# Kernel tuning notes

Measured on AMD Instinct MI355X. Metric: run time of the kernel, lower is better.

The kernel has to match this reference:

```python
import jax, jax.numpy as jnp
import numpy as np

FEATURE_DIM = 256
HEADS = 8


def setup_inputs() -> dict:
    key = jax.random.key(0)
    ks = jax.random.split(key, 9)
    d, h = FEATURE_DIM, HEADS
    b, n = 4, 4096
    s_in = 1.0 / np.sqrt(d)
    s_out = 1.0 / np.sqrt(d * h)
    return {
        "x": jax.random.normal(ks[0], (b, n, d), dtype=jnp.float32),
        "Wq": jax.random.uniform(ks[1], (d, d * h), jnp.float32, -s_in, s_in),
        "bq": jax.random.uniform(ks[2], (d * h,), jnp.float32, -s_in, s_in),
        "Wk": jax.random.uniform(ks[3], (d, d * h), jnp.float32, -s_in, s_in),
        "bk": jax.random.uniform(ks[4], (d * h,), jnp.float32, -s_in, s_in),
        "Wv": jax.random.uniform(ks[5], (d, d * h), jnp.float32, -s_in, s_in),
        "bv": jax.random.uniform(ks[6], (d * h,), jnp.float32, -s_in, s_in),
        "Wo": jax.random.uniform(ks[7], (d * h, d), jnp.float32, -s_out, s_out),
        "bo": jax.random.uniform(ks[8], (d,), jnp.float32, -s_out, s_out),
    }


def reference(x, Wq, bq, Wk, bk, Wv, bv, Wo, bo):
    b, n, d = x.shape
    h = HEADS
    scale = d ** (-0.5)
    # projections: (b, n, h, d) -- note: NO head transpose, matching original
    q = (x @ Wq + bq).reshape(b, n, h, d)
    k = (x @ Wk + bk).reshape(b, n, h, d)
    v = (x @ Wv + bv).reshape(b, n, h, d)
    # attention is head-vs-head per token: (b, n, h, h)
    attn = jnp.einsum("bnhd,bngd->bnhg", q, k) * scale
    attn = jax.nn.softmax(attn, axis=-1)
    out = jnp.einsum("bnhg,bngd->bnhd", attn, v).reshape(b, n, h * d)
    return out @ Wo + bo
```

## Files before the change

### kernel.cpp

```cpp
#include <hip/hip_runtime.h>
#include <hip/hip_bf16.h>
#include <math.h>

typedef __bf16 bf16;
typedef __bf16 bf16x4 __attribute__((ext_vector_type(4)));
typedef __bf16 bf16x8 __attribute__((ext_vector_type(8)));
typedef float f32x4 __attribute__((ext_vector_type(4)));
typedef unsigned int u32;
typedef u32 __attribute__((address_space(1))) gu32;
typedef u32 __attribute__((address_space(3))) lu32;

#define TOK   16384
#define D_    256
#define HD    2048
#define QKVN  6144

#define GLDS16(g, l) __builtin_amdgcn_global_load_lds((gu32*)(g), (lu32*)(l), 16, 0, 0)
#define WAIT_VM(n) __builtin_amdgcn_s_waitcnt(0x0F70 | (n))

__global__ void detect_dtype(const void* __restrict__ x, int* __restrict__ flag)
{
    int lane = threadIdx.x;
    const bf16* xb = (const bf16*)x;
    float m = 0.f;
    for (int i = lane; i < 4096; i += 64) {
        float v = fabsf((float)xb[2 * i]);
        if (!(v < 1e4f)) v = 1e30f;
        m = fmaxf(m, v);
    }
    for (int off = 32; off; off >>= 1) m = fmaxf(m, __shfl_xor(m, off, 64));
    if (lane == 0) *flag = (m > 1e4f) ? 1 : 0;
}

__global__ __launch_bounds__(256) void convert_x(
    const void* __restrict__ src, bf16* __restrict__ dst,
    const int* __restrict__ flag)
{
    int i = blockIdx.x * 256 + threadIdx.x;
    bf16x4 o;
    if (*flag) {
        f32x4 v = ((const f32x4*)src)[i];
        for (int e = 0; e < 4; e++) o[e] = (bf16)v[e];
    } else {
        o = ((const bf16x4*)src)[i];
    }
    ((bf16x4*)dst)[i] = o;
}

__global__ __launch_bounds__(256) void fuse_bias(
    const void* __restrict__ bq, const void* __restrict__ bk,
    const void* __restrict__ bv, const void* __restrict__ bo,
    bf16* __restrict__ bqkv, bf16* __restrict__ bob,
    const int* __restrict__ flag)
{
    int i = blockIdx.x * 256 + threadIdx.x;
    if (i >= 6400) return;
    const void* src; bf16* dst; int off;
    if (i < 2048)      { src = bq; dst = bqkv;        off = i; }
    else if (i < 4096) { src = bk; dst = bqkv + 2048; off = i - 2048; }
    else if (i < 6144) { src = bv; dst = bqkv + 4096; off = i - 4096; }
    else               { src = bo; dst = bob;         off = i - 6144; }
    float v = (*flag) ? ((const float*)src)[off] : (float)((const bf16*)src)[off];
    dst[off] = (bf16)v;
}

__global__ __launch_bounds__(256) void transpose_cvt3(
    const void* __restrict__ Wq, const void* __restrict__ Wk,
    const void* __restrict__ Wv, bf16* __restrict__ WT,
    const int* __restrict__ flag)
{
    __shared__ float tile[32][33];
    int z = blockIdx.z;
    const void* src = (z == 0) ? Wq : (z == 1) ? Wk : Wv;
    bf16* dst = WT + (size_t)z * 2048 * 256;
    int f = *flag;
    int R = 256, C = 2048;
    int tc = blockIdx.x * 32, tr = blockIdx.y * 32;
    int lx = threadIdx.x & 31, ly = threadIdx.x >> 5;
    for (int i = 0; i < 4; i++) {
        int r = ly + i * 8;
        size_t idx = (size_t)(tr + r) * C + tc + lx;
        tile[r][lx] = f ? ((const float*)src)[idx] : (float)((const bf16*)src)[idx];
    }
    __syncthreads();
    for (int i = 0; i < 4; i++) {
        int r = ly + i * 8;
        dst[(size_t)(tc + r) * R + tr + lx] = (bf16)tile[lx][r];
    }
}

__global__ __launch_bounds__(256) void transpose_cvt(
    const void* __restrict__ src, bf16* __restrict__ dst, int R, int C,
    const int* __restrict__ flag)
{
    __shared__ float tile[32][33];
    int f = *flag;
    int tc = blockIdx.x * 32, tr = blockIdx.y * 32;
    int lx = threadIdx.x & 31, ly = threadIdx.x >> 5;
    for (int i = 0; i < 4; i++) {
        int r = ly + i * 8;
        size_t idx = (size_t)(tr + r) * C + tc + lx;
        tile[r][lx] = f ? ((const float*)src)[idx] : (float)((const bf16*)src)[idx];
    }
    __syncthreads();
    for (int i = 0; i < 4; i++) {
        int r = ly + i * 8;
        dst[(size_t)(tc + r) * R + tr + lx] = (bf16)tile[lx][r];
    }
}

__global__ __launch_bounds__(256) void proj_gemm(
    const bf16* __restrict__ X, const bf16* __restrict__ WT,
    const bf16* __restrict__ bqkv, bf16* __restrict__ qkv)
{
    __shared__ char smem[36864];
    bf16* As = (bf16*)smem;
    bf16* Bs = (bf16*)(smem + 16384);
    int m0 = blockIdx.y * 128, n0 = blockIdx.x * 128;
    int tid = threadIdx.x, wave = tid >> 6, lane = tid & 63;
    int wm = (wave >> 1) * 64, wn = (wave & 1) * 64;
    int mrow = lane & 15, quad = lane >> 4;
    int lrow8 = lane >> 3, lslot = lane & 7;

    f32x4 acc[4][4] = {};
    for (int k0 = 0; k0 < D_; k0 += 64) {
        __syncthreads();
        for (int i = 0; i < 4; i++) {
            int rbase = wave * 32 + i * 8;
            int row = rbase + lrow8;
            int gc = lslot ^ (row & 7);
            GLDS16(&X[(size_t)(m0 + row) * D_ + k0 + gc * 8], &As[rbase * 64]);
            GLDS16(&WT[(size_t)(n0 + row) * D_ + k0 + gc * 8], &Bs[rbase * 64]);
        }
        __syncthreads();
        for (int kk = 0; kk < 64; kk += 32) {
            int slot = (((kk >> 3) + quad) ^ (mrow & 7)) * 8;
            bf16x8 af[4], bfv[4];
            for (int mt = 0; mt < 4; mt++)
                af[mt] = *(const bf16x8*)&As[(wm + mt * 16 + mrow) * 64 + slot];
            for (int nt = 0; nt < 4; nt++)
                bfv[nt] = *(const bf16x8*)&Bs[(wn + nt * 16 + mrow) * 64 + slot];
            for (int mt = 0; mt < 4; mt++)
                for (int nt = 0; nt < 4; nt++)
                    acc[mt][nt] = __builtin_amdgcn_mfma_f32_16x16x32_bf16(
                        bfv[nt], af[mt], acc[mt][nt], 0, 0, 0);
        }
    }

    __syncthreads();
    bf16* ep = (bf16*)smem + wave * (64 * 72);
    for (int mt = 0; mt < 4; mt++) {
        for (int nt = 0; nt < 4; nt++) {
            int col = n0 + wn + nt * 16 + quad * 4;
            bf16x4 bb = *(const bf16x4*)&bqkv[col];
            bf16x4 o;
            for (int r = 0; r < 4; r++) o[r] = (bf16)(acc[mt][nt][r] + (float)bb[r]);
            *(bf16x4*)&ep[(mt * 16 + mrow) * 72 + nt * 16 + quad * 4] = o;
        }
    }
    __syncthreads();
    for (int i = 0; i < 8; i++) {
        int r = i * 8 + (lane >> 3);
        int cb = (lane & 7) * 8;
        bf16x8 val = *(const bf16x8*)&ep[r * 72 + cb];
        *(bf16x8*)&qkv[(size_t)(m0 + wm + r) * QKVN + n0 + wn + cb] = val;
    }
}

__global__ __launch_bounds__(256) void attn(bf16* __restrict__ qkv)
{
    __shared__ bf16 sh[4][6144];
    int wave = threadIdx.x >> 6, lane = threadIdx.x & 63;
    bf16* sq = sh[wave];
    int h = lane >> 3, g = lane & 7;
    int wid = blockIdx.x * 4 + wave;
    int start = (wid < 1024) ? wid * 6 : 6144 + (wid - 1024) * 5;
    int count = (wid < 1024) ? 6 : 5;

    for (int ti = 0; ti < count; ti++) {
        int t = start + ti;
        bf16* base = qkv + (size_t)t * QKVN;
        for (int i = 0; i < 12; i++) {
            int s = i * 64 + lane;
            int row = s >> 5, cs = s & 31;
            int gc = cs ^ (row & 7);
            GLDS16(base + row * 256 + gc * 8, (char*)sq + i * 1024);
        }
        WAIT_VM(4);

        const bf16* qrow = sq + h * 256;
        const bf16* krow = sq + (8 + g) * 256;
        float s0 = 0.f, s1 = 0.f, s2 = 0.f, s3 = 0.f;
        for (int c = 0; c < 32; c += 4) {
            bf16x8 a0 = *(const bf16x8*)&qrow[((c + 0) ^ h) * 8];
            bf16x8 b0 = *(const bf16x8*)&krow[((c + 0) ^ g) * 8];
            bf16x8 a1 = *(const bf16x8*)&qrow[((c + 1) ^ h) * 8];
            bf16x8 b1 = *(const bf16x8*)&krow[((c + 1) ^ g) * 8];
            bf16x8 a2 = *(const bf16x8*)&qrow[((c + 2) ^ h) * 8];
            bf16x8 b2 = *(const bf16x8*)&krow[((c + 2) ^ g) * 8];
            bf16x8 a3 = *(const bf16x8*)&qrow[((c + 3) ^ h) * 8];
            bf16x8 b3 = *(const bf16x8*)&krow[((c + 3) ^ g) * 8];
            for (int e = 0; e < 8; e++) {
                s0 += (float)a0[e] * (float)b0[e];
                s1 += (float)a1[e] * (float)b1[e];
                s2 += (float)a2[e] * (float)b2[e];
                s3 += (float)a3[e] * (float)b3[e];
            }
        }
        float s = ((s0 + s1) + (s2 + s3)) * 0.0625f;
        float m = s;
        for (int off = 1; off < 8; off <<= 1) m = fmaxf(m, __shfl_xor(m, off, 8));
        float p = __expf(s - m);
        float sum = p;
        for (int off = 1; off < 8; off <<= 1) sum += __shfl_xor(sum, off, 8);
        p /= sum;

        float pv[8];
        for (int g2 = 0; g2 < 8; g2++) pv[g2] = __shfl(p, h * 8 + g2, 64);

        WAIT_VM(0);

        float acc[4][8] = {};
        for (int g2 = 0; g2 < 8; g2++) {
            float pw = pv[g2];
            const bf16* vrow = sq + (16 + g2) * 256;
            for (int mm = 0; mm < 4; mm++) {
                bf16x8 v = *(const bf16x8*)&vrow[((g ^ g2) + 8 * mm) * 8];
                for (int e = 0; e < 8; e++) acc[mm][e] += pw * (float)v[e];
            }
        }
        bf16* obase = base + h * D_;
        for (int mm = 0; mm < 4; mm++) {
            bf16x8 o;
            for (int e = 0; e < 8; e++) o[e] = (bf16)acc[mm][e];
            *(bf16x8*)&obase[(g + 8 * mm) * 8] = o;
        }
    }
}

__global__ __launch_bounds__(256) void out_gemm(
    const bf16* __restrict__ qkv, const bf16* __restrict__ WoT,
    const bf16* __restrict__ bob, float* __restrict__ outp)
{
    __shared__ bf16 As[64 * 128];
    __shared__ bf16 Bs[128 * 128];
    int m0 = blockIdx.y * 64, n0 = blockIdx.x * 128;
    int tid = threadIdx.x, wave = tid >> 6, lane = tid & 63;
    int wm = (wave >> 1) * 32, wn = (wave & 1) * 64;
    int mrow = lane & 15, quad = lane >> 4;
    int lrow16 = lane >> 4, lslot16 = lane & 15;

    f32x4 acc[2][4] = {};
    for (int k0 = 0; k0 < HD; k0 += 128) {
        __syncthreads();
        for (int i = 0; i < 4; i++) {
            int rbase = wave * 16 + i * 4;
            int row = rbase + lrow16;
            int gc = lslot16 ^ (row & 7);
            GLDS16(&qkv[(size_t)(m0 + row) * QKVN + k0 + gc * 8], &As[rbase * 128]);
        }
        for (int i = 0; i < 8; i++) {
            int rbase = wave * 32 + i * 4;
            int row = rbase + lrow16;
            int gc = lslot16 ^ (row & 7);
            GLDS16(&WoT[(size_t)(n0 + row) * HD + k0 + gc * 8], &Bs[rbase * 128]);
        }
        __syncthreads();
        for (int kk = 0; kk < 128; kk += 32) {
            int slot = (((kk >> 3) + quad) ^ (mrow & 7)) * 8;
            bf16x8 af[2], bfv[4];
            for (int mt = 0; mt < 2; mt++)
                af[mt] = *(const bf16x8*)&As[(wm + mt * 16 + mrow) * 128 + slot];
            for (int nt = 0; nt < 4; nt++)
                bfv[nt] = *(const bf16x8*)&Bs[(wn + nt * 16 + mrow) * 128 + slot];
            for (int mt = 0; mt < 2; mt++)
                for (int nt = 0; nt < 4; nt++)
                    acc[mt][nt] = __builtin_amdgcn_mfma_f32_16x16x32_bf16(
                        bfv[nt], af[mt], acc[mt][nt], 0, 0, 0);
        }
    }

    for (int mt = 0; mt < 2; mt++) {
        int row = m0 + wm + mt * 16 + mrow;
        for (int nt = 0; nt < 4; nt++) {
            int col = n0 + wn + nt * 16 + quad * 4;
            bf16x4 bb = *(const bf16x4*)&bob[col];
            f32x4 o;
            for (int r = 0; r < 4; r++) o[r] = acc[mt][nt][r] + (float)bb[r];
            *(f32x4*)&outp[(size_t)row * D_ + col] = o;
        }
    }
}

extern "C" void kernel_launch(void* const* d_in, const int* in_sizes, int n_in,
                              void* d_out, int out_size, void* d_ws, size_t ws_size,
                              hipStream_t stream)
{
    const void* x  = d_in[0];
    const void* Wq = d_in[1];
    const void* bq = d_in[2];
    const void* Wk = d_in[3];
    const void* bk = d_in[4];
    const void* Wv = d_in[5];
    const void* bv = d_in[6];
    const void* Wo = d_in[7];
    const void* bo = d_in[8];
    float* out = (float*)d_out;

    char* ws = (char*)d_ws;
    bf16* qkv  = (bf16*)ws;
    bf16* WT   = (bf16*)(ws + 201326592);
    bf16* WoT  = (bf16*)(ws + 204472320);
    bf16* xb   = (bf16*)(ws + 205520896);
    bf16* bqkv = (bf16*)(ws + 213909504);
    bf16* bob  = (bf16*)(ws + 213921792);
    int*  flag = (int*)(ws + 213922304);

    detect_dtype<<<1, 64, 0, stream>>>(x, flag);

    convert_x<<<4096, 256, 0, stream>>>(x, xb, flag);
    fuse_bias<<<25, 256, 0, stream>>>(bq, bk, bv, bo, bqkv, bob, flag);
    transpose_cvt3<<<dim3(64, 8, 3), 256, 0, stream>>>(Wq, Wk, Wv, WT, flag);
    transpose_cvt<<<dim3(8, 64), 256, 0, stream>>>(Wo, WoT, 2048, 256, flag);

    proj_gemm<<<dim3(48, 128), 256, 0, stream>>>(xb, WT, bqkv, qkv);
    attn<<<768, 256, 0, stream>>>(qkv);
    out_gemm<<<dim3(2, 256), 256, 0, stream>>>(qkv, WoT, bob, out);
}
```

Measured before the change: 257.3 us.

## Fuse dtype detection and prep kernels into one launch; halve out_gemm M-tile

Merges the dtype-detect, x conversion, bias packing and weight transposes into one prep kernel. Each block redoes a small dtype check in shared memory, which removes four launches and the global flag dependency. Separately, the output GEMM M-tile shrinks from 64 to 32 rows, doubling the grid to 1024 blocks to improve CU occupancy. The cost is twice as many Wo tile loads per output row, and the per-block detection samples only 256 elements instead of 4096.

```diff
diff --git a/kernel.cpp b/kernel.cpp
--- a/kernel.cpp
+++ b/kernel.cpp
@@ -18,64 +18,10 @@
 #define GLDS16(g, l) __builtin_amdgcn_global_load_lds((gu32*)(g), (lu32*)(l), 16, 0, 0)
 #define WAIT_VM(n) __builtin_amdgcn_s_waitcnt(0x0F70 | (n))
 
-__global__ void detect_dtype(const void* __restrict__ x, int* __restrict__ flag)
-{
-    int lane = threadIdx.x;
-    const bf16* xb = (const bf16*)x;
-    float m = 0.f;
-    for (int i = lane; i < 4096; i += 64) {
-        float v = fabsf((float)xb[2 * i]);
-        if (!(v < 1e4f)) v = 1e30f;
-        m = fmaxf(m, v);
-    }
-    for (int off = 32; off; off >>= 1) m = fmaxf(m, __shfl_xor(m, off, 64));
-    if (lane == 0) *flag = (m > 1e4f) ? 1 : 0;
-}
-
-__global__ __launch_bounds__(256) void convert_x(
-    const void* __restrict__ src, bf16* __restrict__ dst,
-    const int* __restrict__ flag)
-{
-    int i = blockIdx.x * 256 + threadIdx.x;
-    bf16x4 o;
-    if (*flag) {
-        f32x4 v = ((const f32x4*)src)[i];
-        for (int e = 0; e < 4; e++) o[e] = (bf16)v[e];
-    } else {
-        o = ((const bf16x4*)src)[i];
-    }
-    ((bf16x4*)dst)[i] = o;
-}
-
-__global__ __launch_bounds__(256) void fuse_bias(
-    const void* __restrict__ bq, const void* __restrict__ bk,
-    const void* __restrict__ bv, const void* __restrict__ bo,
-    bf16* __restrict__ bqkv, bf16* __restrict__ bob,
-    const int* __restrict__ flag)
-{
-    int i = blockIdx.x * 256 + threadIdx.x;
-    if (i >= 6400) return;
-    const void* src; bf16* dst; int off;
-    if (i < 2048)      { src = bq; dst = bqkv;        off = i; }
-    else if (i < 4096) { src = bk; dst = bqkv + 2048; off = i - 2048; }
-    else if (i < 6144) { src = bv; dst = bqkv + 4096; off = i - 4096; }
-    else               { src = bo; dst = bob;         off = i - 6144; }
-    float v = (*flag) ? ((const float*)src)[off] : (float)((const bf16*)src)[off];
-    dst[off] = (bf16)v;
-}
-
-__global__ __launch_bounds__(256) void transpose_cvt3(
-    const void* __restrict__ Wq, const void* __restrict__ Wk,
-    const void* __restrict__ Wv, bf16* __restrict__ WT,
-    const int* __restrict__ flag)
-{
-    __shared__ float tile[32][33];
-    int z = blockIdx.z;
-    const void* src = (z == 0) ? Wq : (z == 1) ? Wk : Wv;
-    bf16* dst = WT + (size_t)z * 2048 * 256;
-    int f = *flag;
-    int R = 256, C = 2048;
-    int tc = blockIdx.x * 32, tr = blockIdx.y * 32;
+__device__ __forceinline__ void transpose_body(
+    const void* __restrict__ src, bf16* __restrict__ dst, int R, int C,
+    int tc, int tr, int f, float (*tile)[33])
+{
     int lx = threadIdx.x & 31, ly = threadIdx.x >> 5;
     for (int i = 0; i < 4; i++) {
         int r = ly + i * 8;
@@ -89,23 +35,57 @@
     }
 }
 
-__global__ __launch_bounds__(256) void transpose_cvt(
-    const void* __restrict__ src, bf16* __restrict__ dst, int R, int C,
-    const int* __restrict__ flag)
+__global__ __launch_bounds__(256) void prep(
+    const void* __restrict__ x,
+    const void* __restrict__ Wq, const void* __restrict__ bq,
+    const void* __restrict__ Wk, const void* __restrict__ bk,
+    const void* __restrict__ Wv, const void* __restrict__ bv,
+    const void* __restrict__ Wo, const void* __restrict__ bo,
+    bf16* __restrict__ xb, bf16* __restrict__ WT, bf16* __restrict__ WoT,
+    bf16* __restrict__ bqkv, bf16* __restrict__ bob)
 {
     __shared__ float tile[32][33];
-    int f = *flag;
-    int tc = blockIdx.x * 32, tr = blockIdx.y * 32;
-    int lx = threadIdx.x & 31, ly = threadIdx.x >> 5;
-    for (int i = 0; i < 4; i++) {
-        int r = ly + i * 8;
-        size_t idx = (size_t)(tr + r) * C + tc + lx;
-        tile[r][lx] = f ? ((const float*)src)[idx] : (float)((const bf16*)src)[idx];
-    }
-    __syncthreads();
-    for (int i = 0; i < 4; i++) {
-        int r = ly + i * 8;
-        dst[(size_t)(tc + r) * R + tr + lx] = (bf16)tile[lx][r];
+    __shared__ int sflag;
+    int tid = threadIdx.x;
+    if (tid == 0) sflag = 0;
+    __syncthreads();
+    {
+        float v = fabsf((float)((const bf16*)x)[2 * tid]);
+        if (!(v < 1e4f)) sflag = 1;
+    }
+    __syncthreads();
+    int f = sflag;
+    int b = blockIdx.x;
+
+    if (b < 4096) {
+        int i = b * 256 + tid;
+        bf16x4 o;
+        if (f) { f32x4 v = ((const f32x4*)x)[i]; for (int e = 0; e < 4; e++) o[e] = (bf16)v[e]; }
+        else   { o = ((const bf16x4*)x)[i]; }
+        ((bf16x4*)xb)[i] = o;
+    } else if (b < 4121) {
+        int i = (b - 4096) * 256 + tid;
+        if (i < 6400) {
+            const void* src; bf16* dst; int off;
+            if (i < 2048)      { src = bq; dst = bqkv;        off = i; }
+            else if (i < 4096) { src = bk; dst = bqkv + 2048; off = i - 2048; }
+            else if (i < 6144) { src = bv; dst = bqkv + 4096; off = i - 4096; }
+            else               { src = bo; dst = bob;         off = i - 6144; }
+            float v = f ? ((const float*)src)[off] : (float)((const bf16*)src)[off];
+            dst[off] = (bf16)v;
+        }
+        __syncthreads();
+    } else if (b < 5657) {
+        int idx = b - 4121;
+        int tx = idx & 63, rest = idx >> 6;
+        int ty = rest & 7, tz = rest >> 3;
+        const void* src = (tz == 0) ? Wq : (tz == 1) ? Wk : Wv;
+        bf16* dst = WT + (size_t)tz * 2048 * 256;
+        transpose_body(src, dst, 256, 2048, tx * 32, ty * 32, f, tile);
+    } else {
+        int idx = b - 5657;
+        int tx = idx & 7, ty = idx >> 3;
+        transpose_body(Wo, WoT, 2048, 256, tx * 32, ty * 32, f, tile);
     }
 }
 
@@ -242,19 +222,19 @@
     const bf16* __restrict__ qkv, const bf16* __restrict__ WoT,
     const bf16* __restrict__ bob, float* __restrict__ outp)
 {
-    __shared__ bf16 As[64 * 128];
+    __shared__ bf16 As[32 * 128];
     __shared__ bf16 Bs[128 * 128];
-    int m0 = blockIdx.y * 64, n0 = blockIdx.x * 128;
+    int m0 = blockIdx.y * 32, n0 = blockIdx.x * 128;
     int tid = threadIdx.x, wave = tid >> 6, lane = tid & 63;
-    int wm = (wave >> 1) * 32, wn = (wave & 1) * 64;
+    int wm = (wave >> 1) * 16, wn = (wave & 1) * 64;
     int mrow = lane & 15, quad = lane >> 4;
     int lrow16 = lane >> 4, lslot16 = lane & 15;
 
-    f32x4 acc[2][4] = {};
+    f32x4 acc[4] = {};
     for (int k0 = 0; k0 < HD; k0 += 128) {
         __syncthreads();
-        for (int i = 0; i < 4; i++) {
-            int rbase = wave * 16 + i * 4;
+        for (int i = 0; i < 2; i++) {
+            int rbase = wave * 8 + i * 4;
             int row = rbase + lrow16;
             int gc = lslot16 ^ (row & 7);
             GLDS16(&qkv[(size_t)(m0 + row) * QKVN + k0 + gc * 8], &As[rbase * 128]);
@@ -268,27 +248,23 @@
         __syncthreads();
         for (int kk = 0; kk < 128; kk += 32) {
             int slot = (((kk >> 3) + quad) ^ (mrow & 7)) * 8;
-            bf16x8 af[2], bfv[4];
-            for (int mt = 0; mt < 2; mt++)
-                af[mt] = *(const bf16x8*)&As[(wm + mt * 16 + mrow) * 128 + slot];
+            bf16x8 af = *(const bf16x8*)&As[(wm + mrow) * 128 + slot];
+            bf16x8 bfv[4];
             for (int nt = 0; nt < 4; nt++)
                 bfv[nt] = *(const bf16x8*)&Bs[(wn + nt * 16 + mrow) * 128 + slot];
-            for (int mt = 0; mt < 2; mt++)
-                for (int nt = 0; nt < 4; nt++)
-                    acc[mt][nt] = __builtin_amdgcn_mfma_f32_16x16x32_bf16(
-                        bfv[nt], af[mt], acc[mt][nt], 0, 0, 0);
-        }
-    }
-
-    for (int mt = 0; mt < 2; mt++) {
-        int row = m0 + wm + mt * 16 + mrow;
-        for (int nt = 0; nt < 4; nt++) {
-            int col = n0 + wn + nt * 16 + quad * 4;
-            bf16x4 bb = *(const bf16x4*)&bob[col];
-            f32x4 o;
-            for (int r = 0; r < 4; r++) o[r] = acc[mt][nt][r] + (float)bb[r];
-            *(f32x4*)&outp[(size_t)row * D_ + col] = o;
-        }
+            for (int nt = 0; nt < 4; nt++)
+                acc[nt] = __builtin_amdgcn_mfma_f32_16x16x32_bf16(
+                    bfv[nt], af, acc[nt], 0, 0, 0);
+        }
+    }
+
+    int row = m0 + wm + mrow;
+    for (int nt = 0; nt < 4; nt++) {
+        int col = n0 + wn + nt * 16 + quad * 4;
+        bf16x4 bb = *(const bf16x4*)&bob[col];
+        f32x4 o;
+        for (int r = 0; r < 4; r++) o[r] = acc[nt][r] + (float)bb[r];
+        *(f32x4*)&outp[(size_t)row * D_ + col] = o;
     }
 }
 
@@ -314,16 +290,10 @@
     bf16* xb   = (bf16*)(ws + 205520896);
     bf16* bqkv = (bf16*)(ws + 213909504);
     bf16* bob  = (bf16*)(ws + 213921792);
-    int*  flag = (int*)(ws + 213922304);
-
-    detect_dtype<<<1, 64, 0, stream>>>(x, flag);
-
-    convert_x<<<4096, 256, 0, stream>>>(x, xb, flag);
-    fuse_bias<<<25, 256, 0, stream>>>(bq, bk, bv, bo, bqkv, bob, flag);
-    transpose_cvt3<<<dim3(64, 8, 3), 256, 0, stream>>>(Wq, Wk, Wv, WT, flag);
-    transpose_cvt<<<dim3(8, 64), 256, 0, stream>>>(Wo, WoT, 2048, 256, flag);
-
+
+    prep<<<6169, 256, 0, stream>>>(x, Wq, bq, Wk, bk, Wv, bv, Wo, bo,
+                                   xb, WT, WoT, bqkv, bob);
     proj_gemm<<<dim3(48, 128), 256, 0, stream>>>(xb, WT, bqkv, qkv);
     attn<<<768, 256, 0, stream>>>(qkv);
-    out_gemm<<<dim3(2, 256), 256, 0, stream>>>(qkv, WoT, bob, out);
-}
+    out_gemm<<<dim3(2, 512), 256, 0, stream>>>(qkv, WoT, bob, out);
+}
```

Measured after the change: 236.6 us. -8.1%, faster.
